# Optimization experiments

Hardware: AMD Instinct MI355X
Metric: run time of the kernel (lower is better)

## Reference

```python
import jax, jax.numpy as jnp
import numpy as np

E = 8          # n_routed_experts
D = 2048       # model dim
I = 1408       # moe_inter_dim
K = 2          # n_activated_experts (top-k)
T = 4096       # num tokens


def setup_inputs() -> dict:
    key = jax.random.key(0)
    k1, k2, k3, k4, k5 = jax.random.split(key, 5)
    x = jax.random.normal(k1, (T, D), dtype=jnp.float32)
    token_mask = jnp.ones((T,), dtype=bool)
    weights = jax.random.uniform(k2, (T, K), dtype=jnp.float32)
    indices = jax.random.randint(k3, (T, K), 0, E)
    init_std = 0.02
    gate_and_up_projs = jax.random.normal(k4, (E, D, 2 * I), dtype=jnp.float32) * init_std
    down_projs = jax.random.normal(k5, (E, I, D), dtype=jnp.float32) * init_std
    return {
        "x": x,
        "token_mask": token_mask,
        "weights": weights,
        "indices": indices,
        "gate_and_up_projs": gate_and_up_projs,
        "down_projs": down_projs,
    }


def reference(x, token_mask, weights, indices, gate_and_up_projs, down_projs):
    # Per-expert gate+up projection over all tokens (dense equivalent of the
    # dispatch + grouped-GEMM): [E, T, 2I]
    gu = jnp.einsum("td,edh->eth", x, gate_and_up_projs)
    gate, up = jnp.split(gu, 2, axis=-1)          # swiglu uses torch.chunk(.., 2, -1)
    inter = jax.nn.silu(gate) * up                # [E, T, I]
    y = jnp.einsum("eti,eid->etd", inter, down_projs)  # [E, T, D]
    # Combine: masked tokens (indices filled to -1) contribute nothing -> zero weight
    w_eff = weights * token_mask[:, None].astype(weights.dtype)   # [T, K]
    tok = jnp.arange(T)
    gathered = y[indices, tok[:, None], :]        # [T, K, D]
    out = jnp.einsum("tk,tkd->td", w_eff, gathered)
    return out.astype(x.dtype)
```

## Files before the change

### kernel.cpp

```cpp
#include <hip/hip_runtime.h>
#include <hip/hip_bf16.h>
#include <cstdint>
#include <cstddef>

#define TT 4096
#define DD 2048
#define II 1408
#define EE 8
#define KK 2
#define H2 2816

#define MAXTILES 72
#define BK 32
#define LDK 40

#define TPE   16
#define NB1   11
#define NB2   16
#define JS1   (TPE * NB1)
#define JS2   (TPE * NB2)
#define GRID1 (EE * JS1)
#define GRID2 (EE * JS2)

#define NCONV 4096
#define NTR1  (44 * 32 * EE)
#define NTR2  (32 * 22 * EE)

typedef __bf16 bf16x8 __attribute__((ext_vector_type(8)));
typedef float  f32x4  __attribute__((ext_vector_type(4)));

static __device__ __forceinline__ unsigned short f2bf(float f) {
    union { float f; unsigned int u; } v; v.f = f;
    unsigned int u = v.u;
    u += 0x7fffu + ((u >> 16) & 1u);
    return (unsigned short)(u >> 16);
}

static __device__ __forceinline__ bf16x8 ld_frag(const unsigned short* p) {
    return *(const bf16x8*)p;
}

static __device__ __forceinline__ void gload16(const unsigned short* g, unsigned short* l) {
    __builtin_amdgcn_global_load_lds(
        (__attribute__((address_space(1))) void*)(g),
        (__attribute__((address_space(3))) void*)(l),
        16, 0, 0);
}

static __device__ __forceinline__ void do_tr_cvt(const float* __restrict__ src,
                                                 unsigned short* __restrict__ dst,
                                                 int K, int H, int bx, int by, int bz,
                                                 char* smem) {
    float (*tile)[65] = (float (*)[65])smem;
    int h0 = bx * 64, k0 = by * 64;
    const float* s = src + (size_t)bz * K * H;
    unsigned short* d = dst + (size_t)bz * K * H;
    int t = threadIdx.x;
    #pragma unroll
    for (int i = 0; i < 4; i++) {
        int idx = t + i * 256;
        int r = idx >> 4, c = (idx & 15) * 4;
        float4 v = *(const float4*)(s + (size_t)(k0 + r) * H + h0 + c);
        tile[r][c] = v.x; tile[r][c + 1] = v.y; tile[r][c + 2] = v.z; tile[r][c + 3] = v.w;
    }
    __syncthreads();
    #pragma unroll
    for (int i = 0; i < 4; i++) {
        int idx = t + i * 256;
        int h = idx >> 4, c = (idx & 15) * 4;
        ushort4 o;
        o.x = f2bf(tile[c][h]);     o.y = f2bf(tile[c + 1][h]);
        o.z = f2bf(tile[c + 2][h]); o.w = f2bf(tile[c + 3][h]);
        *(ushort4*)(d + (size_t)(h0 + h) * K + k0 + c) = o;
    }
}

static __device__ void do_bucket(const int* __restrict__ indices,
                                 const float* __restrict__ weights,
                                 int* __restrict__ ctok, float* __restrict__ cw,
                                 int* __restrict__ tr0, int* __restrict__ trows,
                                 int* __restrict__ te,
                                 int* __restrict__ tb1, int* __restrict__ tb2,
                                 int* __restrict__ inv, char* smem) {
    struct BkS { int cnt[EE]; int nt[EE]; int tb[EE]; int cur[EE]; };
    BkS* s = (BkS*)smem;
    int tid = threadIdx.x;
    if (tid < EE) s->cnt[tid] = 0;
    __syncthreads();
    for (int g = tid; g < TT * KK; g += 256) atomicAdd(&s->cnt[indices[g]], 1);
    __syncthreads();
    if (tid == 0) {
        int off = 0, nt = 0;
        for (int e = 0; e < EE; e++) {
            int c = s->cnt[e];
            s->cur[e] = off;
            s->tb[e] = nt;
            int n = (c + 127) >> 7;
            s->nt[e] = n;
            for (int j = 0; j < n; j++) {
                tr0[nt]   = off + j * 128;
                trows[nt] = min(128, c - j * 128);
                te[nt]    = e;
                nt++;
            }
            off += c;
        }
        for (; nt < MAXTILES; nt++) trows[nt] = 0;
    }
    __syncthreads();
    for (int g = tid; g < GRID1; g += 256) {
        int e = g & 7, j = g >> 3;
        int ntl = s->nt[e], v = -1;
        if (ntl > 0 && j < ntl * NB1) {
            int ti = j % ntl, nb = j / ntl;
            v = ((s->tb[e] + ti) << 5) | nb;
        }
        tb1[g] = v;
    }
    for (int g = tid; g < GRID2; g += 256) {
        int e = g & 7, j = g >> 3;
        int ntl = s->nt[e], v = -1;
        if (ntl > 0 && j < ntl * NB2) {
            int ti = j % ntl, nb = j / ntl;
            v = ((s->tb[e] + ti) << 5) | nb;
        }
        tb2[g] = v;
    }
    __syncthreads();
    if (tid == 0) {
        int c1 = 0, c2 = 0;
        for (int e = 0; e < EE; e++) {
            int ntl = s->nt[e];
            for (int j = JS1; j < ntl * NB1; j++) {
                int ti = j % ntl, nb = j / ntl;
                while (tb1[c1] != -1) c1++;
                tb1[c1] = ((s->tb[e] + ti) << 5) | nb;
            }
            for (int j = JS2; j < ntl * NB2; j++) {
                int ti = j % ntl, nb = j / ntl;
                while (tb2[c2] != -1) c2++;
                tb2[c2] = ((s->tb[e] + ti) << 5) | nb;
            }
        }
    }
    __syncthreads();
    for (int g = tid; g < TT * KK; g += 256) {
        int e = indices[g];
        int pos = atomicAdd(&s->cur[e], 1);
        ctok[pos] = g >> 1;
        cw[pos]   = weights[g];
        inv[g]    = pos;
    }
}

__global__ __launch_bounds__(256) void k_prep(const float* __restrict__ x,
                                              unsigned short* __restrict__ xb,
                                              const float* __restrict__ gup,
                                              unsigned short* __restrict__ wt1,
                                              const int* __restrict__ indices,
                                              const float* __restrict__ weights,
                                              int* __restrict__ ctok, float* __restrict__ cw,
                                              int* __restrict__ tr0, int* __restrict__ trows,
                                              int* __restrict__ te,
                                              int* __restrict__ tb1, int* __restrict__ tb2,
                                              int* __restrict__ inv) {
    __shared__ char smem[16768];
    int b = blockIdx.x;
    if (b == 0) {
        do_bucket(indices, weights, ctok, cw, tr0, trows, te, tb1, tb2, inv, smem);
        return;
    }
    b -= 1;
    if (b < NCONV) {
        size_t i = ((size_t)b * 256 + threadIdx.x) * 8;
        const float4* p = (const float4*)(x + i);
        float4 a = p[0], c = p[1];
        uint4 o;
        o.x = (unsigned)f2bf(a.x) | ((unsigned)f2bf(a.y) << 16);
        o.y = (unsigned)f2bf(a.z) | ((unsigned)f2bf(a.w) << 16);
        o.z = (unsigned)f2bf(c.x) | ((unsigned)f2bf(c.y) << 16);
        o.w = (unsigned)f2bf(c.z) | ((unsigned)f2bf(c.w) << 16);
        *(uint4*)(xb + i) = o;
        return;
    }
    b -= NCONV;
    int bx = b % 44, by = (b / 44) % 32, bz = b / (44 * 32);
    do_tr_cvt(gup, wt1, DD, H2, bx, by, bz, smem);
}


__global__ __launch_bounds__(256, 2) void k_work1(const unsigned short* __restrict__ xb,
                                                  const unsigned short* __restrict__ wt1,
                                                  const int* __restrict__ tbl,
                                                  const int* __restrict__ tr0,
                                                  const int* __restrict__ trows,
                                                  const int* __restrict__ te,
                                                  const int* __restrict__ ctok,
                                                  unsigned short* __restrict__ inter,
                                                  const float* __restrict__ down,
                                                  unsigned short* __restrict__ wt2) {
    __shared__ char smem[49664];
    if (blockIdx.x >= GRID1) {
        int b = blockIdx.x - GRID1;
        int bx = b % 32, by = (b / 32) % 22, bz = b / (32 * 22);
        do_tr_cvt(down, wt2, II, DD, bx, by, bz, smem);
        return;
    }
    unsigned short* As = (unsigned short*)smem;
    unsigned short* Bg = (unsigned short*)(smem + 16384);
    unsigned short* Bu = (unsigned short*)(smem + 32768);
    int* toks = (int*)(smem + 49152);

    int ent = tbl[blockIdx.x];
    if (ent < 0) return;
    int tile = ent >> 5;
    int rows = trows[tile];
    int row0 = tr0[tile], e = te[tile], n0 = (ent & 31) * 128;
    int tid = threadIdx.x, wave = tid >> 6, lane = tid & 63;

    for (int i = tid; i < 128; i += 256) toks[i] = ctok[row0 + ((i < rows) ? i : 0)];
    __syncthreads();

    int rl = wave * 32 + (lane >> 2);
    int kc = (lane & 3) * 8;
    const unsigned short* gA0 = xb + (size_t)toks[rl] * DD + kc;
    const unsigned short* gA1 = xb + (size_t)toks[rl + 16] * DD + kc;
    const unsigned short* wte = wt1 + (size_t)e * H2 * DD;
    const unsigned short* gBg0 = wte + (size_t)(n0 + rl) * DD + kc;
    const unsigned short* gBg1 = wte + (size_t)(n0 + rl + 16) * DD + kc;
    const unsigned short* gBu0 = gBg0 + (size_t)II * DD;
    const unsigned short* gBu1 = gBg1 + (size_t)II * DD;

    unsigned lr0 = (unsigned)(wave * 32) * 32;
    unsigned lr1 = (unsigned)(wave * 32 + 16) * 32;

    int mb = (wave & 1) * 64, nb = (wave >> 1) * 64;
    int lrow = lane & 15, quad = lane >> 4;

    f32x4 accg[4][4], accu[4][4];
    #pragma unroll
    for (int i = 0; i < 4; i++)
        #pragma unroll
        for (int j = 0; j < 4; j++) { accg[i][j] = (f32x4){0,0,0,0}; accu[i][j] = (f32x4){0,0,0,0}; }

    gload16(gA0,  &As[lr0]); gload16(gA1,  &As[lr1]);
    gload16(gBg0, &Bg[lr0]); gload16(gBg1, &Bg[lr1]);
    gload16(gBu0, &Bu[lr0]); gload16(gBu1, &Bu[lr1]);
    gA0 += BK; gA1 += BK; gBg0 += BK; gBg1 += BK; gBu0 += BK; gBu1 += BK;

    int cur = 0;
    #pragma unroll 1
    for (int k0 = 0; k0 < DD; k0 += BK) {
        __syncthreads();
        if (k0 + BK < DD) {
            unsigned nx = (unsigned)(cur ^ 1) * 4096;
            gload16(gA0,  &As[nx + lr0]); gload16(gA1,  &As[nx + lr1]);
            gload16(gBg0, &Bg[nx + lr0]); gload16(gBg1, &Bg[nx + lr1]);
            gload16(gBu0, &Bu[nx + lr0]); gload16(gBu1, &Bu[nx + lr1]);
            gA0 += BK; gA1 += BK; gBg0 += BK; gBg1 += BK; gBu0 += BK; gBu1 += BK;
        }

        unsigned cb = (unsigned)cur * 4096;
        bf16x8 af[4], bg[4], bu[4];
        #pragma unroll
        for (int i = 0; i < 4; i++)
            af[i] = ld_frag(&As[cb + (mb + i * 16 + lrow) * 32 + quad * 8]);
        #pragma unroll
        for (int j = 0; j < 4; j++) {
            bg[j] = ld_frag(&Bg[cb + (nb + j * 16 + lrow) * 32 + quad * 8]);
            bu[j] = ld_frag(&Bu[cb + (nb + j * 16 + lrow) * 32 + quad * 8]);
        }
        #pragma unroll
        for (int i = 0; i < 4; i++)
            #pragma unroll
            for (int j = 0; j < 4; j++) {
                accg[i][j] = __builtin_amdgcn_mfma_f32_16x16x32_bf16(af[i], bg[j], accg[i][j], 0, 0, 0);
                accu[i][j] = __builtin_amdgcn_mfma_f32_16x16x32_bf16(af[i], bu[j], accu[i][j], 0, 0, 0);
            }
        cur ^= 1;
    }

    #pragma unroll
    for (int i = 0; i < 4; i++) {
        int rl0 = mb + i * 16 + quad * 4;
        #pragma unroll
        for (int r = 0; r < 4; r++) {
            int rr = rl0 + r;
            if (rr < rows) {
                size_t base = (size_t)(row0 + rr) * II + n0 + nb;
                #pragma unroll
                for (int j = 0; j < 4; j++) {
                    float g = accg[i][j][r], u = accu[i][j][r];
                    float s = g / (1.0f + __expf(-g));
                    inter[base + j * 16 + lrow] = f2bf(s * u);
                }
            }
        }
    }
}

__global__ __launch_bounds__(256, 2) void k_gemm2_f(const unsigned short* __restrict__ inter,
                                                    const unsigned short* __restrict__ wt2,
                                                    const int* __restrict__ tbl,
                                                    const int* __restrict__ tr0,
                                                    const int* __restrict__ trows,
                                                    const int* __restrict__ te,
                                                    float* __restrict__ y) {
    int ent = tbl[blockIdx.x];
    if (ent < 0) return;
    int tile = ent >> 5;
    int rows = trows[tile];
    int row0 = tr0[tile], e = te[tile], n0 = (ent & 31) * 128;
    int tid = threadIdx.x, wave = tid >> 6, lane = tid & 63;

    __shared__ unsigned short As[2][128 * 32];
    __shared__ unsigned short Bs[2][128 * 32];

    int rl = wave * 32 + (lane >> 2);
    int kc = (lane & 3) * 8;
    int r0c = (rl < rows) ? rl : 0;
    int r1c = (rl + 16 < rows) ? rl + 16 : 0;
    const unsigned short* gA0 = inter + (size_t)(row0 + r0c) * II + kc;
    const unsigned short* gA1 = inter + (size_t)(row0 + r1c) * II + kc;
    const unsigned short* wte = wt2 + (size_t)e * DD * II;
    const unsigned short* gB0 = wte + (size_t)(n0 + rl) * II + kc;
    const unsigned short* gB1 = wte + (size_t)(n0 + rl + 16) * II + kc;

    unsigned lr0 = (unsigned)(wave * 32) * 32;
    unsigned lr1 = (unsigned)(wave * 32 + 16) * 32;

    int mb = (wave & 1) * 64, nb = (wave >> 1) * 64;
    int lrow = lane & 15, quad = lane >> 4;

    f32x4 acc[4][4];
    #pragma unroll
    for (int i = 0; i < 4; i++)
        #pragma unroll
        for (int j = 0; j < 4; j++) acc[i][j] = (f32x4){0,0,0,0};

    gload16(gA0, &As[0][lr0]); gload16(gA1, &As[0][lr1]);
    gload16(gB0, &Bs[0][lr0]); gload16(gB1, &Bs[0][lr1]);
    gA0 += BK; gA1 += BK; gB0 += BK; gB1 += BK;

    int cur = 0;
    #pragma unroll 1
    for (int k0 = 0; k0 < II; k0 += BK) {
        __syncthreads();
        if (k0 + BK < II) {
            int nx = cur ^ 1;
            gload16(gA0, &As[nx][lr0]); gload16(gA1, &As[nx][lr1]);
            gload16(gB0, &Bs[nx][lr0]); gload16(gB1, &Bs[nx][lr1]);
            gA0 += BK; gA1 += BK; gB0 += BK; gB1 += BK;
        }

        bf16x8 af[4], bfg[4];
        #pragma unroll
        for (int i = 0; i < 4; i++)
            af[i] = ld_frag(&As[cur][(mb + i * 16 + lrow) * 32 + quad * 8]);
        #pragma unroll
        for (int j = 0; j < 4; j++)
            bfg[j] = ld_frag(&Bs[cur][(nb + j * 16 + lrow) * 32 + quad * 8]);
        #pragma unroll
        for (int i = 0; i < 4; i++)
            #pragma unroll
            for (int j = 0; j < 4; j++)
                acc[i][j] = __builtin_amdgcn_mfma_f32_16x16x32_bf16(af[i], bfg[j], acc[i][j], 0, 0, 0);
        cur ^= 1;
    }

    #pragma unroll
    for (int i = 0; i < 4; i++) {
        int rl0 = mb + i * 16 + quad * 4;
        #pragma unroll
        for (int r = 0; r < 4; r++) {
            int rr = rl0 + r;
            if (rr < rows) {
                float* yp = y + (size_t)(row0 + rr) * DD + n0 + nb;
                #pragma unroll
                for (int j = 0; j < 4; j++)
                    yp[j * 16 + lrow] = acc[i][j][r];
            }
        }
    }
}

__global__ __launch_bounds__(256) void k_combine(const float* __restrict__ y,
                                                 const int* __restrict__ inv,
                                                 const float* __restrict__ weights,
                                                 float* __restrict__ out) {
    int t = blockIdx.x;
    int d0 = threadIdx.x * 8;
    int p0 = inv[t * 2], p1 = inv[t * 2 + 1];
    float w0 = weights[t * 2], w1 = weights[t * 2 + 1];
    const float4* a = (const float4*)(y + (size_t)p0 * DD + d0);
    const float4* b = (const float4*)(y + (size_t)p1 * DD + d0);
    float4 a0 = a[0], a1 = a[1], b0 = b[0], b1 = b[1];
    float4 o0, o1;
    o0.x = w0 * a0.x + w1 * b0.x; o0.y = w0 * a0.y + w1 * b0.y;
    o0.z = w0 * a0.z + w1 * b0.z; o0.w = w0 * a0.w + w1 * b0.w;
    o1.x = w0 * a1.x + w1 * b1.x; o1.y = w0 * a1.y + w1 * b1.y;
    o1.z = w0 * a1.z + w1 * b1.z; o1.w = w0 * a1.w + w1 * b1.w;
    float4* op = (float4*)(out + (size_t)t * DD + d0);
    op[0] = o0; op[1] = o1;
}


__global__ __launch_bounds__(256, 2) void k_gemm1_s(const unsigned short* __restrict__ xb,
                                                    const float* __restrict__ gup,
                                                    const int* __restrict__ tr0,
                                                    const int* __restrict__ trows,
                                                    const int* __restrict__ te,
                                                    const int* __restrict__ ctok,
                                                    unsigned short* __restrict__ inter) {
    int tile = blockIdx.x;
    int rows = trows[tile];
    if (rows == 0) return;
    int row0 = tr0[tile];
    int e    = te[tile];
    int n0   = blockIdx.y * 128;
    int tid  = threadIdx.x;

    __shared__ unsigned short As[128 * LDK];
    __shared__ unsigned short Bg[128 * LDK];
    __shared__ unsigned short Bu[128 * LDK];
    __shared__ int toks[128];

    for (int i = tid; i < 128; i += 256) toks[i] = (i < rows) ? ctok[row0 + i] : -1;

    const float* Wbase = gup + (size_t)e * DD * H2;

    int wave = tid >> 6, lane = tid & 63;
    int mb = (wave & 1) * 64, nb = (wave >> 1) * 64;
    int lrow = lane & 15, quad = lane >> 4;

    f32x4 accg[4][4], accu[4][4];
    #pragma unroll
    for (int i = 0; i < 4; i++)
        #pragma unroll
        for (int j = 0; j < 4; j++) { accg[i][j] = (f32x4){0,0,0,0}; accu[i][j] = (f32x4){0,0,0,0}; }

    #pragma unroll 1
    for (int k0 = 0; k0 < DD; k0 += BK) {
        __syncthreads();
        #pragma unroll
        for (int c = tid; c < 512; c += 256) {
            int r = c >> 2, kk = (c & 3) << 3;
            uint4 v = make_uint4(0, 0, 0, 0);
            int t = toks[r];
            if (t >= 0) v = *(const uint4*)(xb + (size_t)t * DD + k0 + kk);
            *(uint4*)&As[r * LDK + kk] = v;
        }
        #pragma unroll
        for (int c = tid; c < 512; c += 256) {
            int n = c & 127, kcc = (c >> 7) << 3;
            const float* p = Wbase + (size_t)(k0 + kcc) * H2 + (n0 + n);
            unsigned short hg[8], hu[8];
            #pragma unroll
            for (int j = 0; j < 8; j++) {
                hg[j] = f2bf(p[(size_t)j * H2]);
                hu[j] = f2bf(p[(size_t)j * H2 + II]);
            }
            uint4 vg, vu;
            vg.x = (unsigned)hg[0] | ((unsigned)hg[1] << 16);
            vg.y = (unsigned)hg[2] | ((unsigned)hg[3] << 16);
            vg.z = (unsigned)hg[4] | ((unsigned)hg[5] << 16);
            vg.w = (unsigned)hg[6] | ((unsigned)hg[7] << 16);
            vu.x = (unsigned)hu[0] | ((unsigned)hu[1] << 16);
            vu.y = (unsigned)hu[2] | ((unsigned)hu[3] << 16);
            vu.z = (unsigned)hu[4] | ((unsigned)hu[5] << 16);
            vu.w = (unsigned)hu[6] | ((unsigned)hu[7] << 16);
            *(uint4*)&Bg[n * LDK + kcc] = vg;
            *(uint4*)&Bu[n * LDK + kcc] = vu;
        }
        __syncthreads();

        bf16x8 af[4], bg[4], bu[4];
        #pragma unroll
        for (int i = 0; i < 4; i++)
            af[i] = ld_frag(&As[(mb + i * 16 + lrow) * LDK + quad * 8]);
        #pragma unroll
        for (int j = 0; j < 4; j++) {
            bg[j] = ld_frag(&Bg[(nb + j * 16 + lrow) * LDK + quad * 8]);
            bu[j] = ld_frag(&Bu[(nb + j * 16 + lrow) * LDK + quad * 8]);
        }
        #pragma unroll
        for (int i = 0; i < 4; i++)
            #pragma unroll
            for (int j = 0; j < 4; j++) {
                accg[i][j] = __builtin_amdgcn_mfma_f32_16x16x32_bf16(af[i], bg[j], accg[i][j], 0, 0, 0);
                accu[i][j] = __builtin_amdgcn_mfma_f32_16x16x32_bf16(af[i], bu[j], accu[i][j], 0, 0, 0);
            }
    }

    #pragma unroll
    for (int i = 0; i < 4; i++) {
        int rl0 = mb + i * 16 + quad * 4;
        #pragma unroll
        for (int r = 0; r < 4; r++) {
            int rl = rl0 + r;
            if (rl < rows) {
                size_t base = (size_t)(row0 + rl) * II + n0 + nb;
                #pragma unroll
                for (int j = 0; j < 4; j++) {
                    float g = accg[i][j][r], u = accu[i][j][r];
                    float s = g / (1.0f + __expf(-g));
                    inter[base + j * 16 + lrow] = f2bf(s * u);
                }
            }
        }
    }
}

__global__ __launch_bounds__(256, 2) void k_gemm2_s(const unsigned short* __restrict__ inter,
                                                    const float* __restrict__ down,
                                                    const int* __restrict__ tr0,
                                                    const int* __restrict__ trows,
                                                    const int* __restrict__ te,
                                                    const int* __restrict__ ctok,
                                                    const float* __restrict__ cw,
                                                    float* __restrict__ out) {
    int tile = blockIdx.x;
    int rows = trows[tile];
    if (rows == 0) return;
    int row0 = tr0[tile];
    int e    = te[tile];
    int n0   = blockIdx.y * 128;
    int tid  = threadIdx.x;

    __shared__ unsigned short As[128 * LDK];
    __shared__ unsigned short Bs[128 * LDK];
    __shared__ int   toks[128];
    __shared__ float wts[128];

    for (int i = tid; i < 128; i += 256) {
        bool v = (i < rows);
        toks[i] = v ? ctok[row0 + i] : -1;
        wts[i]  = v ? cw[row0 + i] : 0.0f;
    }

    const float* Wbase = down + (size_t)e * II * DD;

    int wave = tid >> 6, lane = tid & 63;
    int mb = (wave & 1) * 64, nb = (wave >> 1) * 64;
    int lrow = lane & 15, quad = lane >> 4;

    f32x4 acc[4][4];
    #pragma unroll
    for (int i = 0; i < 4; i++)
        #pragma unroll
        for (int j = 0; j < 4; j++) acc[i][j] = (f32x4){0,0,0,0};

    #pragma unroll 1
    for (int k0 = 0; k0 < II; k0 += BK) {
        __syncthreads();
        #pragma unroll
        for (int c = tid; c < 512; c += 256) {
            int r = c >> 2, kk = (c & 3) << 3;
            uint4 v = make_uint4(0, 0, 0, 0);
            if (r < rows) v = *(const uint4*)(inter + (size_t)(row0 + r) * II + k0 + kk);
            *(uint4*)&As[r * LDK + kk] = v;
        }
        #pragma unroll
        for (int c = tid; c < 512; c += 256) {
            int n = c & 127, kcc = (c >> 7) << 3;
            const float* p = Wbase + (size_t)(k0 + kcc) * DD + (n0 + n);
            unsigned short h[8];
            #pragma unroll
            for (int j = 0; j < 8; j++) h[j] = f2bf(p[(size_t)j * DD]);
            uint4 v;
            v.x = (unsigned)h[0] | ((unsigned)h[1] << 16);
            v.y = (unsigned)h[2] | ((unsigned)h[3] << 16);
            v.z = (unsigned)h[4] | ((unsigned)h[5] << 16);
            v.w = (unsigned)h[6] | ((unsigned)h[7] << 16);
            *(uint4*)&Bs[n * LDK + kcc] = v;
        }
        __syncthreads();

        bf16x8 af[4], bfg[4];
        #pragma unroll
        for (int i = 0; i < 4; i++)
            af[i] = ld_frag(&As[(mb + i * 16 + lrow) * LDK + quad * 8]);
        #pragma unroll
        for (int j = 0; j < 4; j++)
            bfg[j] = ld_frag(&Bs[(nb + j * 16 + lrow) * LDK + quad * 8]);
        #pragma unroll
        for (int i = 0; i < 4; i++)
            #pragma unroll
            for (int j = 0; j < 4; j++)
                acc[i][j] = __builtin_amdgcn_mfma_f32_16x16x32_bf16(af[i], bfg[j], acc[i][j], 0, 0, 0);
    }

    #pragma unroll
    for (int i = 0; i < 4; i++) {
        int rl0 = mb + i * 16 + quad * 4;
        #pragma unroll
        for (int r = 0; r < 4; r++) {
            int rl = rl0 + r;
            if (rl < rows) {
                int t = toks[rl];
                float w = wts[rl];
                float* op = out + (size_t)t * DD + n0 + nb;
                #pragma unroll
                for (int j = 0; j < 4; j++)
                    unsafeAtomicAdd(op + j * 16 + lrow, w * acc[i][j][r]);
            }
        }
    }
}

constexpr size_t OFF_CNT   = 0;
constexpr size_t OFF_CUR   = 64;
constexpr size_t OFF_CTOK  = 256;
constexpr size_t OFF_CW    = OFF_CTOK + (size_t)TT * KK * 4;
constexpr size_t OFF_TR0   = OFF_CW + (size_t)TT * KK * 4;
constexpr size_t OFF_TRS   = OFF_TR0 + 512;
constexpr size_t OFF_TE    = OFF_TRS + 512;
constexpr size_t OFF_TB1   = OFF_TE + 512;
constexpr size_t OFF_TB2   = OFF_TB1 + 8192;
constexpr size_t OFF_INV   = OFF_TB2 + 8192;
constexpr size_t OFF_XB    = (OFF_INV + (size_t)TT * KK * 4 + 255) & ~(size_t)255;
constexpr size_t OFF_INTER = OFF_XB + (size_t)TT * DD * 2;
constexpr size_t OFF_WT1   = OFF_INTER + (size_t)TT * KK * II * 2;
constexpr size_t OFF_WT2   = OFF_WT1 + (size_t)EE * H2 * DD * 2;
constexpr size_t WS_SLOW   = OFF_WT1;
constexpr size_t WS_FAST   = OFF_WT2 + (size_t)EE * DD * II * 2;

extern "C" void kernel_launch(void* const* d_in, const int* in_sizes, int n_in,
                              void* d_out, int out_size, void* d_ws, size_t ws_size,
                              hipStream_t stream) {
    const float* x       = (const float*)d_in[0];
    const float* weights = (const float*)d_in[2];
    const int*   indices = (const int*)d_in[3];
    const float* gup     = (const float*)d_in[4];
    const float* down    = (const float*)d_in[5];
    float* out = (float*)d_out;

    if (ws_size < WS_SLOW) return;

    char* ws = (char*)d_ws;
    int*            ctok     = (int*)(ws + OFF_CTOK);
    float*          cw       = (float*)(ws + OFF_CW);
    int*            tr0      = (int*)(ws + OFF_TR0);
    int*            trows    = (int*)(ws + OFF_TRS);
    int*            te       = (int*)(ws + OFF_TE);
    int*            tb1      = (int*)(ws + OFF_TB1);
    int*            tb2      = (int*)(ws + OFF_TB2);
    int*            inv      = (int*)(ws + OFF_INV);
    unsigned short* xb       = (unsigned short*)(ws + OFF_XB);
    unsigned short* inter    = (unsigned short*)(ws + OFF_INTER);
    unsigned short* wt1      = (unsigned short*)(ws + OFF_WT1);
    unsigned short* wt2      = (unsigned short*)(ws + OFF_WT2);
    float*          y        = (float*)(ws + OFF_WT1);

    if (ws_size >= WS_FAST) {
        k_prep  <<<dim3(1 + NCONV + NTR1), 256, 0, stream>>>(x, xb, gup, wt1,
                     indices, weights, ctok, cw, tr0, trows, te, tb1, tb2, inv);
        k_work1 <<<dim3(GRID1 + NTR2), 256, 0, stream>>>(xb, wt1, tb1, tr0, trows,
                     te, ctok, inter, down, wt2);
        k_gemm2_f<<<dim3(GRID2), 256, 0, stream>>>(inter, wt2, tb2, tr0, trows, te, y);
        k_combine<<<dim3(TT), 256, 0, stream>>>(y, inv, weights, out);
    } else {
        hipMemsetAsync(d_out, 0, (size_t)TT * DD * sizeof(float), stream);
        k_prep  <<<dim3(1 + NCONV), 256, 0, stream>>>(x, xb, gup, wt1,
                     indices, weights, ctok, cw, tr0, trows, te, tb1, tb2, inv);
        k_gemm1_s<<<dim3(MAXTILES, II / 128), 256, 0, stream>>>(xb, gup, tr0, trows, te, ctok, inter);
        k_gemm2_s<<<dim3(MAXTILES, DD / 128), 256, 0, stream>>>(inter, down, tr0, trows, te, ctok, cw, out);
    }
}
```

Before: 573.8 us.

## Use 512-thread blocks with 8 waves in both expert GEMM kernels

Doubles the threads per block in k_work1 and k_gemm2_f from 256 to 512. Each wave now owns a 64x32 output sub-tile instead of 64x64 and issues one async LDS load per operand instead of two. The transpose helper becomes a stride loop over blockDim. The aim is to cut accumulator registers per wave and raise the number of resident waves to hide memory latency, at the cost of less fragment reuse per wave and more LDS reads per MFMA.

```diff
diff --git a/kernel.cpp b/kernel.cpp
--- a/kernel.cpp
+++ b/kernel.cpp
@@ -55,18 +55,13 @@
     int h0 = bx * 64, k0 = by * 64;
     const float* s = src + (size_t)bz * K * H;
     unsigned short* d = dst + (size_t)bz * K * H;
-    int t = threadIdx.x;
-    #pragma unroll
-    for (int i = 0; i < 4; i++) {
-        int idx = t + i * 256;
+    for (int idx = threadIdx.x; idx < 1024; idx += blockDim.x) {
         int r = idx >> 4, c = (idx & 15) * 4;
         float4 v = *(const float4*)(s + (size_t)(k0 + r) * H + h0 + c);
         tile[r][c] = v.x; tile[r][c + 1] = v.y; tile[r][c + 2] = v.z; tile[r][c + 3] = v.w;
     }
     __syncthreads();
-    #pragma unroll
-    for (int i = 0; i < 4; i++) {
-        int idx = t + i * 256;
+    for (int idx = threadIdx.x; idx < 1024; idx += blockDim.x) {
         int h = idx >> 4, c = (idx & 15) * 4;
         ushort4 o;
         o.x = f2bf(tile[c][h]);     o.y = f2bf(tile[c + 1][h]);
@@ -189,7 +184,7 @@
 }
 
 
-__global__ __launch_bounds__(256, 2) void k_work1(const unsigned short* __restrict__ xb,
+__global__ __launch_bounds__(512, 6) void k_work1(const unsigned short* __restrict__ xb,
                                                   const unsigned short* __restrict__ wt1,
                                                   const int* __restrict__ tbl,
                                                   const int* __restrict__ tr0,
@@ -218,35 +213,29 @@
     int row0 = tr0[tile], e = te[tile], n0 = (ent & 31) * 128;
     int tid = threadIdx.x, wave = tid >> 6, lane = tid & 63;
 
-    for (int i = tid; i < 128; i += 256) toks[i] = ctok[row0 + ((i < rows) ? i : 0)];
+    for (int i = tid; i < 128; i += 512) toks[i] = ctok[row0 + ((i < rows) ? i : 0)];
     __syncthreads();
 
-    int rl = wave * 32 + (lane >> 2);
+    int rl = wave * 16 + (lane >> 2);
     int kc = (lane & 3) * 8;
-    const unsigned short* gA0 = xb + (size_t)toks[rl] * DD + kc;
-    const unsigned short* gA1 = xb + (size_t)toks[rl + 16] * DD + kc;
+    const unsigned short* gA  = xb + (size_t)toks[rl] * DD + kc;
     const unsigned short* wte = wt1 + (size_t)e * H2 * DD;
-    const unsigned short* gBg0 = wte + (size_t)(n0 + rl) * DD + kc;
-    const unsigned short* gBg1 = wte + (size_t)(n0 + rl + 16) * DD + kc;
-    const unsigned short* gBu0 = gBg0 + (size_t)II * DD;
-    const unsigned short* gBu1 = gBg1 + (size_t)II * DD;
-
-    unsigned lr0 = (unsigned)(wave * 32) * 32;
-    unsigned lr1 = (unsigned)(wave * 32 + 16) * 32;
-
-    int mb = (wave & 1) * 64, nb = (wave >> 1) * 64;
+    const unsigned short* gBg = wte + (size_t)(n0 + rl) * DD + kc;
+    const unsigned short* gBu = gBg + (size_t)II * DD;
+
+    unsigned lr = (unsigned)(wave * 16) * 32;
+
+    int mb = (wave & 1) * 64, nb = (wave >> 1) * 32;
     int lrow = lane & 15, quad = lane >> 4;
 
-    f32x4 accg[4][4], accu[4][4];
+    f32x4 accg[4][2], accu[4][2];
     #pragma unroll
     for (int i = 0; i < 4; i++)
         #pragma unroll
-        for (int j = 0; j < 4; j++) { accg[i][j] = (f32x4){0,0,0,0}; accu[i][j] = (f32x4){0,0,0,0}; }
-
-    gload16(gA0,  &As[lr0]); gload16(gA1,  &As[lr1]);
-    gload16(gBg0, &Bg[lr0]); gload16(gBg1, &Bg[lr1]);
-    gload16(gBu0, &Bu[lr0]); gload16(gBu1, &Bu[lr1]);
-    gA0 += BK; gA1 += BK; gBg0 += BK; gBg1 += BK; gBu0 += BK; gBu1 += BK;
+        for (int j = 0; j < 2; j++) { accg[i][j] = (f32x4){0,0,0,0}; accu[i][j] = (f32x4){0,0,0,0}; }
+
+    gload16(gA, &As[lr]); gload16(gBg, &Bg[lr]); gload16(gBu, &Bu[lr]);
+    gA += BK; gBg += BK; gBu += BK;
 
     int cur = 0;
     #pragma unroll 1
@@ -254,26 +243,24 @@
         __syncthreads();
         if (k0 + BK < DD) {
             unsigned nx = (unsigned)(cur ^ 1) * 4096;
-            gload16(gA0,  &As[nx + lr0]); gload16(gA1,  &As[nx + lr1]);
-            gload16(gBg0, &Bg[nx + lr0]); gload16(gBg1, &Bg[nx + lr1]);
-            gload16(gBu0, &Bu[nx + lr0]); gload16(gBu1, &Bu[nx + lr1]);
-            gA0 += BK; gA1 += BK; gBg0 += BK; gBg1 += BK; gBu0 += BK; gBu1 += BK;
+            gload16(gA, &As[nx + lr]); gload16(gBg, &Bg[nx + lr]); gload16(gBu, &Bu[nx + lr]);
+            gA += BK; gBg += BK; gBu += BK;
         }
 
         unsigned cb = (unsigned)cur * 4096;
-        bf16x8 af[4], bg[4], bu[4];
+        bf16x8 af[4], bg[2], bu[2];
         #pragma unroll
         for (int i = 0; i < 4; i++)
             af[i] = ld_frag(&As[cb + (mb + i * 16 + lrow) * 32 + quad * 8]);
         #pragma unroll
-        for (int j = 0; j < 4; j++) {
+        for (int j = 0; j < 2; j++) {
             bg[j] = ld_frag(&Bg[cb + (nb + j * 16 + lrow) * 32 + quad * 8]);
             bu[j] = ld_frag(&Bu[cb + (nb + j * 16 + lrow) * 32 + quad * 8]);
         }
         #pragma unroll
         for (int i = 0; i < 4; i++)
             #pragma unroll
-            for (int j = 0; j < 4; j++) {
+            for (int j = 0; j < 2; j++) {
                 accg[i][j] = __builtin_amdgcn_mfma_f32_16x16x32_bf16(af[i], bg[j], accg[i][j], 0, 0, 0);
                 accu[i][j] = __builtin_amdgcn_mfma_f32_16x16x32_bf16(af[i], bu[j], accu[i][j], 0, 0, 0);
             }
@@ -289,7 +276,7 @@
             if (rr < rows) {
                 size_t base = (size_t)(row0 + rr) * II + n0 + nb;
                 #pragma unroll
-                for (int j = 0; j < 4; j++) {
+                for (int j = 0; j < 2; j++) {
                     float g = accg[i][j][r], u = accu[i][j][r];
                     float s = g / (1.0f + __expf(-g));
                     inter[base + j * 16 + lrow] = f2bf(s * u);
@@ -299,7 +286,7 @@
     }
 }
 
-__global__ __launch_bounds__(256, 2) void k_gemm2_f(const unsigned short* __restrict__ inter,
+__global__ __launch_bounds__(512, 8) void k_gemm2_f(const unsigned short* __restrict__ inter,
                                                     const unsigned short* __restrict__ wt2,
                                                     const int* __restrict__ tbl,
                                                     const int* __restrict__ tr0,
@@ -316,31 +303,26 @@
     __shared__ unsigned short As[2][128 * 32];
     __shared__ unsigned short Bs[2][128 * 32];
 
-    int rl = wave * 32 + (lane >> 2);
+    int rl = wave * 16 + (lane >> 2);
     int kc = (lane & 3) * 8;
-    int r0c = (rl < rows) ? rl : 0;
-    int r1c = (rl + 16 < rows) ? rl + 16 : 0;
-    const unsigned short* gA0 = inter + (size_t)(row0 + r0c) * II + kc;
-    const unsigned short* gA1 = inter + (size_t)(row0 + r1c) * II + kc;
+    int rc = (rl < rows) ? rl : 0;
+    const unsigned short* gA  = inter + (size_t)(row0 + rc) * II + kc;
     const unsigned short* wte = wt2 + (size_t)e * DD * II;
-    const unsigned short* gB0 = wte + (size_t)(n0 + rl) * II + kc;
-    const unsigned short* gB1 = wte + (size_t)(n0 + rl + 16) * II + kc;
-
-    unsigned lr0 = (unsigned)(wave * 32) * 32;
-    unsigned lr1 = (unsigned)(wave * 32 + 16) * 32;
-
-    int mb = (wave & 1) * 64, nb = (wave >> 1) * 64;
+    const unsigned short* gB  = wte + (size_t)(n0 + rl) * II + kc;
+
+    unsigned lr = (unsigned)(wave * 16) * 32;
+
+    int mb = (wave & 1) * 64, nb = (wave >> 1) * 32;
     int lrow = lane & 15, quad = lane >> 4;
 
-    f32x4 acc[4][4];
+    f32x4 acc[4][2];
     #pragma unroll
     for (int i = 0; i < 4; i++)
         #pragma unroll
-        for (int j = 0; j < 4; j++) acc[i][j] = (f32x4){0,0,0,0};
-
-    gload16(gA0, &As[0][lr0]); gload16(gA1, &As[0][lr1]);
-    gload16(gB0, &Bs[0][lr0]); gload16(gB1, &Bs[0][lr1]);
-    gA0 += BK; gA1 += BK; gB0 += BK; gB1 += BK;
+        for (int j = 0; j < 2; j++) acc[i][j] = (f32x4){0,0,0,0};
+
+    gload16(gA, &As[0][lr]); gload16(gB, &Bs[0][lr]);
+    gA += BK; gB += BK;
 
     int cur = 0;
     #pragma unroll 1
@@ -348,22 +330,21 @@
         __syncthreads();
         if (k0 + BK < II) {
             int nx = cur ^ 1;
-            gload16(gA0, &As[nx][lr0]); gload16(gA1, &As[nx][lr1]);
-            gload16(gB0, &Bs[nx][lr0]); gload16(gB1, &Bs[nx][lr1]);
-            gA0 += BK; gA1 += BK; gB0 += BK; gB1 += BK;
-        }
-
-        bf16x8 af[4], bfg[4];
+            gload16(gA, &As[nx][lr]); gload16(gB, &Bs[nx][lr]);
+            gA += BK; gB += BK;
+        }
+
+        bf16x8 af[4], bfg[2];
         #pragma unroll
         for (int i = 0; i < 4; i++)
             af[i] = ld_frag(&As[cur][(mb + i * 16 + lrow) * 32 + quad * 8]);
         #pragma unroll
-        for (int j = 0; j < 4; j++)
+        for (int j = 0; j < 2; j++)
             bfg[j] = ld_frag(&Bs[cur][(nb + j * 16 + lrow) * 32 + quad * 8]);
         #pragma unroll
         for (int i = 0; i < 4; i++)
             #pragma unroll
-            for (int j = 0; j < 4; j++)
+            for (int j = 0; j < 2; j++)
                 acc[i][j] = __builtin_amdgcn_mfma_f32_16x16x32_bf16(af[i], bfg[j], acc[i][j], 0, 0, 0);
         cur ^= 1;
     }
@@ -377,7 +358,7 @@
             if (rr < rows) {
                 float* yp = y + (size_t)(row0 + rr) * DD + n0 + nb;
                 #pragma unroll
-                for (int j = 0; j < 4; j++)
+                for (int j = 0; j < 2; j++)
                     yp[j * 16 + lrow] = acc[i][j][r];
             }
         }
@@ -608,8 +589,6 @@
     }
 }
 
-constexpr size_t OFF_CNT   = 0;
-constexpr size_t OFF_CUR   = 64;
 constexpr size_t OFF_CTOK  = 256;
 constexpr size_t OFF_CW    = OFF_CTOK + (size_t)TT * KK * 4;
 constexpr size_t OFF_TR0   = OFF_CW + (size_t)TT * KK * 4;
@@ -655,9 +634,9 @@
     if (ws_size >= WS_FAST) {
         k_prep  <<<dim3(1 + NCONV + NTR1), 256, 0, stream>>>(x, xb, gup, wt1,
                      indices, weights, ctok, cw, tr0, trows, te, tb1, tb2, inv);
-        k_work1 <<<dim3(GRID1 + NTR2), 256, 0, stream>>>(xb, wt1, tb1, tr0, trows,
+        k_work1 <<<dim3(GRID1 + NTR2), 512, 0, stream>>>(xb, wt1, tb1, tr0, trows,
                      te, ctok, inter, down, wt2);
-        k_gemm2_f<<<dim3(GRID2), 256, 0, stream>>>(inter, wt2, tb2, tr0, trows, te, y);
+        k_gemm2_f<<<dim3(GRID2), 512, 0, stream>>>(inter, wt2, tb2, tr0, trows, te, y);
         k_combine<<<dim3(TT), 256, 0, stream>>>(y, inv, weights, out);
     } else {
         hipMemsetAsync(d_out, 0, (size_t)TT * DD * sizeof(float), stream);
```

Result: slower. 1.215 ms (+111.9%).
